# Optimization experiments

Hardware: AMD Instinct MI355X
Metric: run time of the kernel (lower is better)

## Reference

```python
import jax, jax.numpy as jnp
import numpy as np

N, D, F = 8192, 256, 64

def setup_inputs() -> dict:
    key = jax.random.key(0)
    ks = jax.random.split(key, 7)
    s = 0.02
    return {
        "x":  jax.random.normal(ks[0], (N, D), dtype=jnp.float32),
        "Wk": jax.random.normal(ks[1], (F, D), dtype=jnp.float32) * s,
        "bk": jax.random.normal(ks[2], (F,), dtype=jnp.float32) * s,
        "Wv": jax.random.normal(ks[3], (F, D), dtype=jnp.float32) * s,
        "bv": jax.random.normal(ks[4], (F,), dtype=jnp.float32) * s,
        "Wq": jax.random.normal(ks[5], (N, F, D), dtype=jnp.float32) * s,
        "bq": jax.random.normal(ks[6], (N, F), dtype=jnp.float32) * s,
    }

def reference(x, Wk, bk, Wv, bv, Wq, bq):
    # Shared K/V projections: (N, D) -> (N, F)
    k = x @ Wk.T + bk
    v = x @ Wv.T + bv
    # Per-node Q: node i uses its own weight Wq[i] on its own row x[i]
    q = jnp.einsum("nd,nfd->nf", x, Wq) + bq  # (N, F)
    # Scaled dot-product attention over nodes
    scale = 1.0 / jnp.sqrt(jnp.asarray(F, dtype=x.dtype))
    scores = (q @ k.T) * scale               # (N, N)
    attn = jax.nn.softmax(scores, axis=-1)
    return attn @ v                           # (N, F)
```

## Files before the change

### kernel.cpp

```cpp
#include <hip/hip_runtime.h>
#include <math.h>

#define NN 8192
#define DD 256
#define FF 64

#define QSC (0.125f * 1.4426950408889634f)

typedef __attribute__((ext_vector_type(8))) __bf16 bf16x8;
typedef __attribute__((ext_vector_type(4))) __bf16 bf16x4;
typedef __attribute__((ext_vector_type(4))) float f32x4;

static __device__ __forceinline__ f32x4 mfma16(bf16x8 a, bf16x8 b, f32x4 c) {
    return __builtin_amdgcn_mfma_f32_16x16x32_bf16(a, b, c, 0, 0, 0);
}

__global__ __launch_bounds__(256) void proj_q_kernel(
    const float* __restrict__ x, const float* __restrict__ Wq,
    const float* __restrict__ bq, __bf16* __restrict__ q_bf)
{
    __shared__ float T[4][64 * 17];

    const int i = blockIdx.x;
    const int l = threadIdx.x & 63;
    const int w = threadIdx.x >> 6;

    const float4 xf = reinterpret_cast<const float4*>(x)[(size_t)i * 64 + l];
    const float4* wq4 = reinterpret_cast<const float4*>(Wq) + (size_t)i * 4096;

    float pf[16];
#pragma unroll
    for (int ff = 0; ff < 16; ++ff) {
        const int f = w * 16 + ff;
        float4 a = wq4[f * 64 + l];
        pf[ff] = a.x * xf.x + a.y * xf.y + a.z * xf.z + a.w * xf.w;
    }
#pragma unroll
    for (int ff = 0; ff < 16; ++ff) T[w][l * 17 + ff] = pf[ff];
    const int f = l & 15;
    const int c = l >> 4;
    float s = 0.f;
#pragma unroll
    for (int j = 0; j < 16; ++j) s += T[w][(c * 16 + j) * 17 + f];
    s += __shfl_xor(s, 16, 64);
    s += __shfl_xor(s, 32, 64);
    if (l < 16)
        q_bf[(size_t)i * FF + w * 16 + l] =
            (__bf16)((s + bq[(size_t)i * FF + w * 16 + l]) * QSC);
}

__global__ __launch_bounds__(256) void proj_kv_kernel(
    const float* __restrict__ x, const float* __restrict__ Wk,
    const float* __restrict__ bk, const float* __restrict__ Wv,
    const float* __restrict__ bv,
    __bf16* __restrict__ k_bf, __bf16* __restrict__ vT)
{
    const int lane = threadIdx.x & 63;
    const int wave = threadIdx.x >> 6;
    const int g = lane >> 4;
    const int qc = lane & 15;
    const int i0 = blockIdx.x * 64 + wave * 16;

    f32x4 ack[4], acv[4];
#pragma unroll
    for (int nt = 0; nt < 4; ++nt) {
        ack[nt] = (f32x4){0.f, 0.f, 0.f, 0.f};
        acv[nt] = (f32x4){0.f, 0.f, 0.f, 0.f};
    }

    const float4* x4 = reinterpret_cast<const float4*>(x);
#pragma unroll
    for (int ks = 0; ks < 8; ++ks) {
        float4 xa = x4[(size_t)(i0 + qc) * 64 + ks * 8 + g * 2];
        float4 xb = x4[(size_t)(i0 + qc) * 64 + ks * 8 + g * 2 + 1];
        bf16x8 af;
        af[0] = (__bf16)xa.x; af[1] = (__bf16)xa.y; af[2] = (__bf16)xa.z; af[3] = (__bf16)xa.w;
        af[4] = (__bf16)xb.x; af[5] = (__bf16)xb.y; af[6] = (__bf16)xb.z; af[7] = (__bf16)xb.w;
#pragma unroll
        for (int nt = 0; nt < 4; ++nt) {
            const float* wkp = Wk + (size_t)(nt * 16 + qc) * DD + ks * 32 + g * 8;
            const float* wvp = Wv + (size_t)(nt * 16 + qc) * DD + ks * 32 + g * 8;
            float4 wa = reinterpret_cast<const float4*>(wkp)[0];
            float4 wb = reinterpret_cast<const float4*>(wkp)[1];
            bf16x8 bk8;
            bk8[0] = (__bf16)wa.x; bk8[1] = (__bf16)wa.y; bk8[2] = (__bf16)wa.z; bk8[3] = (__bf16)wa.w;
            bk8[4] = (__bf16)wb.x; bk8[5] = (__bf16)wb.y; bk8[6] = (__bf16)wb.z; bk8[7] = (__bf16)wb.w;
            ack[nt] = mfma16(af, bk8, ack[nt]);
            float4 va = reinterpret_cast<const float4*>(wvp)[0];
            float4 vb = reinterpret_cast<const float4*>(wvp)[1];
            bf16x8 bv8;
            bv8[0] = (__bf16)va.x; bv8[1] = (__bf16)va.y; bv8[2] = (__bf16)va.z; bv8[3] = (__bf16)va.w;
            bv8[4] = (__bf16)vb.x; bv8[5] = (__bf16)vb.y; bv8[6] = (__bf16)vb.z; bv8[7] = (__bf16)vb.w;
            acv[nt] = mfma16(af, bv8, acv[nt]);
        }
    }

#pragma unroll
    for (int nt = 0; nt < 4; ++nt) {
        const int f = nt * 16 + qc;
        const float bkf = bk[f];
        const float bvf = bv[f];
#pragma unroll
        for (int r = 0; r < 4; ++r) {
            const int i = i0 + g * 4 + r;
            k_bf[(size_t)i * FF + f] = (__bf16)(ack[nt][r] + bkf);
            vT[(size_t)f * NN + i]   = (__bf16)(acv[nt][r] + bvf);
        }
    }
}

__global__ __launch_bounds__(256) void attn_kernel(
    const __bf16* __restrict__ q_bf, const __bf16* __restrict__ k_bf,
    const __bf16* __restrict__ vT,
    float* __restrict__ Om, float* __restrict__ m_arr, float* __restrict__ l_arr,
    int kv_per_split)
{
    __shared__ __align__(16) __bf16 Klds[64 * 64];
    __shared__ __align__(16) __bf16 Vlds[64 * 64];
    __shared__ __align__(16) __bf16 pT[4][16 * 64];

    const int t = threadIdx.x;
    const int lane = t & 63;
    const int wave = t >> 6;
    const int g = lane >> 4;
    const int qc = lane & 15;
    const int q0 = blockIdx.x * 64 + wave * 16;
    const int s  = blockIdx.y;
    const int qrow = q0 + qc;
    const int sw = qc & 7;

    const int srow = t >> 2;
    const int sbp  = (t & 3) * 2;

    const bf16x8 qf0 = *reinterpret_cast<const bf16x8*>(q_bf + (size_t)qrow * FF + g * 8);
    const bf16x8 qf1 = *reinterpret_cast<const bf16x8*>(q_bf + (size_t)qrow * FF + 32 + g * 8);

    f32x4 o[4];
#pragma unroll
    for (int m = 0; m < 4; ++m) o[m] = (f32x4){0.f, 0.f, 0.f, 0.f};
    float mrun = -INFINITY;
    float lrun = 0.f;

    const int kv0 = s * kv_per_split;

    for (int kb = kv0; kb < kv0 + kv_per_split; kb += 64) {
        __syncthreads();
        {
            const __bf16* src = k_bf + (size_t)(kb + srow) * FF + sbp * 8;
            bf16x8 u0 = *reinterpret_cast<const bf16x8*>(src);
            bf16x8 u1 = *reinterpret_cast<const bf16x8*>(src + 8);
            *reinterpret_cast<bf16x8*>(&Klds[srow * 64 + ((sbp ^ (srow & 7)) * 8)]) = u0;
            *reinterpret_cast<bf16x8*>(&Klds[srow * 64 + (((sbp + 1) ^ (srow & 7)) * 8)]) = u1;
            const __bf16* sv = vT + (size_t)srow * NN + kb + sbp * 8;
            bf16x8 w0 = *reinterpret_cast<const bf16x8*>(sv);
            bf16x8 w1 = *reinterpret_cast<const bf16x8*>(sv + 8);
            *reinterpret_cast<bf16x8*>(&Vlds[srow * 64 + ((sbp ^ (srow & 7)) * 8)]) = w0;
            *reinterpret_cast<bf16x8*>(&Vlds[srow * 64 + (((sbp + 1) ^ (srow & 7)) * 8)]) = w1;
        }
        __syncthreads();

        f32x4 sc[4];
#pragma unroll
        for (int kt = 0; kt < 4; ++kt) {
            const int row = kt * 16 + qc;
            bf16x8 a0 = *reinterpret_cast<const bf16x8*>(&Klds[row * 64 + ((g ^ (qc & 7)) * 8)]);
            bf16x8 a1 = *reinterpret_cast<const bf16x8*>(&Klds[row * 64 + (((4 + g) ^ (qc & 7)) * 8)]);
            f32x4 acc = (f32x4){0.f, 0.f, 0.f, 0.f};
            acc = mfma16(a0, qf0, acc);
            acc = mfma16(a1, qf1, acc);
            sc[kt] = acc;
        }

        float mt = sc[0].x;
#pragma unroll
        for (int kt = 0; kt < 4; ++kt) {
            mt = fmaxf(mt, sc[kt].x); mt = fmaxf(mt, sc[kt].y);
            mt = fmaxf(mt, sc[kt].z); mt = fmaxf(mt, sc[kt].w);
        }
        mt = fmaxf(mt, __shfl_xor(mt, 16, 64));
        mt = fmaxf(mt, __shfl_xor(mt, 32, 64));
        const float mnew = fmaxf(mrun, mt);
        const float alpha = __builtin_amdgcn_exp2f(mrun - mnew);

        float psum = 0.f;
#pragma unroll
        for (int kt = 0; kt < 4; ++kt) {
            float p0 = __builtin_amdgcn_exp2f(sc[kt].x - mnew);
            float p1 = __builtin_amdgcn_exp2f(sc[kt].y - mnew);
            float p2 = __builtin_amdgcn_exp2f(sc[kt].z - mnew);
            float p3 = __builtin_amdgcn_exp2f(sc[kt].w - mnew);
            psum += (p0 + p1) + (p2 + p3);
            bf16x4 pv;
            pv[0] = (__bf16)p0; pv[1] = (__bf16)p1;
            pv[2] = (__bf16)p2; pv[3] = (__bf16)p3;
            const int b = kt * 2 + (g >> 1);
            *reinterpret_cast<bf16x4*>(&pT[wave][qc * 64 + ((b ^ sw) << 3) + (g & 1) * 4]) = pv;
        }
        psum += __shfl_xor(psum, 16, 64);
        psum += __shfl_xor(psum, 32, 64);
        lrun = lrun * alpha + psum;
        mrun = mnew;
#pragma unroll
        for (int m = 0; m < 4; ++m) o[m] *= alpha;

#pragma unroll
        for (int kk = 0; kk < 2; ++kk) {
            const int br = kk * 4 + g;
            bf16x8 pb = *reinterpret_cast<const bf16x8*>(&pT[wave][qc * 64 + ((br ^ sw) << 3)]);
#pragma unroll
            for (int m = 0; m < 4; ++m) {
                const int row = m * 16 + qc;
                bf16x8 a = *reinterpret_cast<const bf16x8*>(
                    &Vlds[row * 64 + (((kk * 4 + g) ^ (qc & 7)) * 8)]);
                o[m] = mfma16(a, pb, o[m]);
            }
        }
    }

    float* op = Om + (size_t)s * FF * NN;
#pragma unroll
    for (int m = 0; m < 4; ++m) {
        op[(size_t)(m * 16 + g * 4 + 0) * NN + q0 + qc] = o[m].x;
        op[(size_t)(m * 16 + g * 4 + 1) * NN + q0 + qc] = o[m].y;
        op[(size_t)(m * 16 + g * 4 + 2) * NN + q0 + qc] = o[m].z;
        op[(size_t)(m * 16 + g * 4 + 3) * NN + q0 + qc] = o[m].w;
    }
    if (g == 0) {
        m_arr[s * NN + qrow] = mrun;
        l_arr[s * NN + qrow] = lrun;
    }
}

__global__ __launch_bounds__(256) void combine_kernel(
    const float* __restrict__ Om, const float* __restrict__ m_arr,
    const float* __restrict__ l_arr, float* __restrict__ out, int nsplit)
{
    const int idx = blockIdx.x * 256 + threadIdx.x;
    const int f = idx >> 13;
    const int i = idx & (NN - 1);

    float M = -INFINITY;
    for (int s = 0; s < nsplit; ++s) M = fmaxf(M, m_arr[s * NN + i]);
    float L = 0.f, acc = 0.f;
    for (int s = 0; s < nsplit; ++s) {
        float wgt = __builtin_amdgcn_exp2f(m_arr[s * NN + i] - M);
        L   += wgt * l_arr[s * NN + i];
        acc += wgt * Om[((size_t)s * FF + f) * NN + i];
    }
    out[(size_t)i * FF + f] = acc / L;
}

extern "C" void kernel_launch(void* const* d_in, const int* in_sizes, int n_in,
                              void* d_out, int out_size, void* d_ws, size_t ws_size,
                              hipStream_t stream) {
    const float* x  = (const float*)d_in[0];
    const float* Wk = (const float*)d_in[1];
    const float* bk = (const float*)d_in[2];
    const float* Wv = (const float*)d_in[3];
    const float* bv = (const float*)d_in[4];
    const float* Wq = (const float*)d_in[5];
    const float* bq = (const float*)d_in[6];
    float* out = (float*)d_out;

    const int nsplit = (ws_size >= (size_t)20971520) ? 8 : 4;
    const int kv_per_split = NN / nsplit;

    char* ws = (char*)d_ws;
    __bf16* q_bf = (__bf16*)(ws);
    __bf16* k_bf = (__bf16*)(ws + ((size_t)1 << 20));
    __bf16* vT   = (__bf16*)(ws + ((size_t)2 << 20));
    float*  Om   = (float*)(ws + ((size_t)3 << 20));
    float*  m_a  = (float*)(ws + ((size_t)3 << 20) + (size_t)nsplit * FF * NN * 4);
    float*  l_a  = (float*)((char*)m_a + (size_t)nsplit * NN * 4);

    hipLaunchKernelGGL(proj_q_kernel, dim3(NN), dim3(256), 0, stream,
                       x, Wq, bq, q_bf);
    hipLaunchKernelGGL(proj_kv_kernel, dim3(NN / 64), dim3(256), 0, stream,
                       x, Wk, bk, Wv, bv, k_bf, vT);
    hipLaunchKernelGGL(attn_kernel, dim3(NN / 64, nsplit), dim3(256), 0, stream,
                       q_bf, k_bf, vT, Om, m_a, l_a, kv_per_split);
    hipLaunchKernelGGL(combine_kernel, dim3(NN * FF / 256), dim3(256), 0, stream,
                       Om, m_a, l_a, out, nsplit);
}
```

Measured before the change: 766.7 us.

## Double-buffer K/V tiles with register prefetch, lazy rescale, and MFMA priority

Splits the K/V shared-memory tiles into two buffers. The next tile is loaded from global memory into registers before the current tile is computed, then written to the other buffer, so only one barrier per iteration remains. It also adds a lazy online-softmax rescale that skips updating the running max unless any lane's max grows by more than a threshold, which removes per-iteration exp and multiply work. s_setprio raises wave priority around the MFMA sections. The cost is twice the LDS footprint, which may lower occupancy, plus a slight numerical-range risk from the deferred rescale.

```diff
diff --git a/kernel.cpp b/kernel.cpp
--- a/kernel.cpp
+++ b/kernel.cpp
@@ -115,8 +115,8 @@
     float* __restrict__ Om, float* __restrict__ m_arr, float* __restrict__ l_arr,
     int kv_per_split)
 {
-    __shared__ __align__(16) __bf16 Klds[64 * 64];
-    __shared__ __align__(16) __bf16 Vlds[64 * 64];
+    __shared__ __align__(16) __bf16 Klds[2][64 * 64];
+    __shared__ __align__(16) __bf16 Vlds[2][64 * 64];
     __shared__ __align__(16) __bf16 pT[4][16 * 64];
 
     const int t = threadIdx.x;
@@ -131,6 +131,8 @@
 
     const int srow = t >> 2;
     const int sbp  = (t & 3) * 2;
+    const int so0 = srow * 64 + ((sbp ^ (srow & 7)) * 8);
+    const int so1 = srow * 64 + (((sbp + 1) ^ (srow & 7)) * 8);
 
     const bf16x8 qf0 = *reinterpret_cast<const bf16x8*>(q_bf + (size_t)qrow * FF + g * 8);
     const bf16x8 qf1 = *reinterpret_cast<const bf16x8*>(q_bf + (size_t)qrow * FF + 32 + g * 8);
@@ -142,53 +144,70 @@
     float lrun = 0.f;
 
     const int kv0 = s * kv_per_split;
-
-    for (int kb = kv0; kb < kv0 + kv_per_split; kb += 64) {
-        __syncthreads();
-        {
-            const __bf16* src = k_bf + (size_t)(kb + srow) * FF + sbp * 8;
-            bf16x8 u0 = *reinterpret_cast<const bf16x8*>(src);
-            bf16x8 u1 = *reinterpret_cast<const bf16x8*>(src + 8);
-            *reinterpret_cast<bf16x8*>(&Klds[srow * 64 + ((sbp ^ (srow & 7)) * 8)]) = u0;
-            *reinterpret_cast<bf16x8*>(&Klds[srow * 64 + (((sbp + 1) ^ (srow & 7)) * 8)]) = u1;
-            const __bf16* sv = vT + (size_t)srow * NN + kb + sbp * 8;
-            bf16x8 w0 = *reinterpret_cast<const bf16x8*>(sv);
-            bf16x8 w1 = *reinterpret_cast<const bf16x8*>(sv + 8);
-            *reinterpret_cast<bf16x8*>(&Vlds[srow * 64 + ((sbp ^ (srow & 7)) * 8)]) = w0;
-            *reinterpret_cast<bf16x8*>(&Vlds[srow * 64 + (((sbp + 1) ^ (srow & 7)) * 8)]) = w1;
-        }
-        __syncthreads();
+    const int niter = kv_per_split >> 6;
+
+    const __bf16* ksrc = k_bf + (size_t)srow * FF + sbp * 8;
+    const __bf16* vsrc = vT  + (size_t)srow * NN + sbp * 8;
+
+    bf16x8 u0 = *reinterpret_cast<const bf16x8*>(ksrc + (size_t)kv0 * FF);
+    bf16x8 u1 = *reinterpret_cast<const bf16x8*>(ksrc + (size_t)kv0 * FF + 8);
+    bf16x8 w0 = *reinterpret_cast<const bf16x8*>(vsrc + kv0);
+    bf16x8 w1 = *reinterpret_cast<const bf16x8*>(vsrc + kv0 + 8);
+    *reinterpret_cast<bf16x8*>(&Klds[0][so0]) = u0;
+    *reinterpret_cast<bf16x8*>(&Klds[0][so1]) = u1;
+    *reinterpret_cast<bf16x8*>(&Vlds[0][so0]) = w0;
+    *reinterpret_cast<bf16x8*>(&Vlds[0][so1]) = w1;
+    __syncthreads();
+
+    for (int it = 0; it < niter; ++it) {
+        const int cur = it & 1;
+        const int itn = (it + 1 < niter) ? (it + 1) : it;
+        const int kbn = kv0 + itn * 64;
+        u0 = *reinterpret_cast<const bf16x8*>(ksrc + (size_t)kbn * FF);
+        u1 = *reinterpret_cast<const bf16x8*>(ksrc + (size_t)kbn * FF + 8);
+        w0 = *reinterpret_cast<const bf16x8*>(vsrc + kbn);
+        w1 = *reinterpret_cast<const bf16x8*>(vsrc + kbn + 8);
+
+        const __bf16* Kb = &Klds[cur][0];
+        const __bf16* Vb = &Vlds[cur][0];
 
         f32x4 sc[4];
+        __builtin_amdgcn_s_setprio(1);
 #pragma unroll
         for (int kt = 0; kt < 4; ++kt) {
             const int row = kt * 16 + qc;
-            bf16x8 a0 = *reinterpret_cast<const bf16x8*>(&Klds[row * 64 + ((g ^ (qc & 7)) * 8)]);
-            bf16x8 a1 = *reinterpret_cast<const bf16x8*>(&Klds[row * 64 + (((4 + g) ^ (qc & 7)) * 8)]);
+            bf16x8 a0 = *reinterpret_cast<const bf16x8*>(&Kb[row * 64 + ((g ^ sw) * 8)]);
+            bf16x8 a1 = *reinterpret_cast<const bf16x8*>(&Kb[row * 64 + (((4 + g) ^ sw) * 8)]);
             f32x4 acc = (f32x4){0.f, 0.f, 0.f, 0.f};
             acc = mfma16(a0, qf0, acc);
             acc = mfma16(a1, qf1, acc);
             sc[kt] = acc;
         }
-
-        float mt = sc[0].x;
-#pragma unroll
-        for (int kt = 0; kt < 4; ++kt) {
-            mt = fmaxf(mt, sc[kt].x); mt = fmaxf(mt, sc[kt].y);
-            mt = fmaxf(mt, sc[kt].z); mt = fmaxf(mt, sc[kt].w);
-        }
+        __builtin_amdgcn_s_setprio(0);
+
+        float mt = fmaxf(fmaxf(sc[0].x, sc[0].y), fmaxf(sc[0].z, sc[0].w));
+#pragma unroll
+        for (int kt = 1; kt < 4; ++kt)
+            mt = fmaxf(mt, fmaxf(fmaxf(sc[kt].x, sc[kt].y), fmaxf(sc[kt].z, sc[kt].w)));
         mt = fmaxf(mt, __shfl_xor(mt, 16, 64));
         mt = fmaxf(mt, __shfl_xor(mt, 32, 64));
-        const float mnew = fmaxf(mrun, mt);
-        const float alpha = __builtin_amdgcn_exp2f(mrun - mnew);
+
+        if (!__all(mt - mrun <= 10.0f)) {
+            const float mnew = fmaxf(mrun, mt);
+            const float alpha = __builtin_amdgcn_exp2f(mrun - mnew);
+            lrun *= alpha;
+#pragma unroll
+            for (int m = 0; m < 4; ++m) o[m] *= alpha;
+            mrun = mnew;
+        }
 
         float psum = 0.f;
 #pragma unroll
         for (int kt = 0; kt < 4; ++kt) {
-            float p0 = __builtin_amdgcn_exp2f(sc[kt].x - mnew);
-            float p1 = __builtin_amdgcn_exp2f(sc[kt].y - mnew);
-            float p2 = __builtin_amdgcn_exp2f(sc[kt].z - mnew);
-            float p3 = __builtin_amdgcn_exp2f(sc[kt].w - mnew);
+            float p0 = __builtin_amdgcn_exp2f(sc[kt].x - mrun);
+            float p1 = __builtin_amdgcn_exp2f(sc[kt].y - mrun);
+            float p2 = __builtin_amdgcn_exp2f(sc[kt].z - mrun);
+            float p3 = __builtin_amdgcn_exp2f(sc[kt].w - mrun);
             psum += (p0 + p1) + (p2 + p3);
             bf16x4 pv;
             pv[0] = (__bf16)p0; pv[1] = (__bf16)p1;
@@ -198,11 +217,9 @@
         }
         psum += __shfl_xor(psum, 16, 64);
         psum += __shfl_xor(psum, 32, 64);
-        lrun = lrun * alpha + psum;
-        mrun = mnew;
-#pragma unroll
-        for (int m = 0; m < 4; ++m) o[m] *= alpha;
-
+        lrun += psum;
+
+        __builtin_amdgcn_s_setprio(1);
 #pragma unroll
         for (int kk = 0; kk < 2; ++kk) {
             const int br = kk * 4 + g;
@@ -211,10 +228,17 @@
             for (int m = 0; m < 4; ++m) {
                 const int row = m * 16 + qc;
                 bf16x8 a = *reinterpret_cast<const bf16x8*>(
-                    &Vlds[row * 64 + (((kk * 4 + g) ^ (qc & 7)) * 8)]);
+                    &Vb[row * 64 + ((br ^ sw) * 8)]);
                 o[m] = mfma16(a, pb, o[m]);
             }
         }
+        __builtin_amdgcn_s_setprio(0);
+
+        *reinterpret_cast<bf16x8*>(&Klds[cur ^ 1][so0]) = u0;
+        *reinterpret_cast<bf16x8*>(&Klds[cur ^ 1][so1]) = u1;
+        *reinterpret_cast<bf16x8*>(&Vlds[cur ^ 1][so0]) = w0;
+        *reinterpret_cast<bf16x8*>(&Vlds[cur ^ 1][so1]) = w1;
+        __syncthreads();
     }
 
     float* op = Om + (size_t)s * FF * NN;
```

New measurement: 765.2 us. About the same (-0.2%).
